# Kernel optimization log

Measured on AMD Instinct MI355X. Metric: run time of the kernel, lower is better.

The kernel has to match this reference:

```python
import jax, jax.numpy as jnp
import numpy as np

H = 4096          # hidden_size
I = 11008         # intermediate_size
G = 128           # AWQ group_size
# AWQ interleaved nibble order within each packed int32
_ORDER = jnp.array([0, 4, 1, 5, 2, 6, 3, 7], dtype=jnp.int32) * 4


def _mk_lin(key, K, N):
    k1, k2, k3 = jax.random.split(key, 3)
    qw = jax.random.randint(k1, (K, N // 8), 0, 100, dtype=jnp.int32)
    qz = jax.random.randint(k2, (K // G, N // 8), 0, 100, dtype=jnp.int32)
    sc = jax.random.normal(k3, (K // G, N), dtype=jnp.float32) * 0.02
    return qw, qz, sc


def setup_inputs() -> dict:
    key = jax.random.key(0)
    ks = jax.random.split(key, 7)
    x = jax.random.normal(ks[0], (8, 16, H), dtype=jnp.float32)
    ln1_w = jnp.ones((H,), dtype=jnp.float32)
    ln2_w = jnp.ones((H,), dtype=jnp.float32)
    qkv_qw, qkv_qz, qkv_sc = _mk_lin(ks[1], H, 3 * H)
    o_qw, o_qz, o_sc = _mk_lin(ks[2], H, H)
    gu_qw, gu_qz, gu_sc = _mk_lin(ks[3], H, 2 * I)
    dn_qw, dn_qz, dn_sc = _mk_lin(ks[4], I, H)
    return dict(x=x, ln1_w=ln1_w, ln2_w=ln2_w,
                qkv_qw=qkv_qw, qkv_qz=qkv_qz, qkv_sc=qkv_sc,
                o_qw=o_qw, o_qz=o_qz, o_sc=o_sc,
                gu_qw=gu_qw, gu_qz=gu_qz, gu_sc=gu_sc,
                dn_qw=dn_qw, dn_qz=dn_qz, dn_sc=dn_sc)


def rmsnorm(x, w, eps=1e-6):
    return x * jax.lax.rsqrt(jnp.mean(x * x, axis=-1, keepdims=True) + eps) * w


def dequant(qw, qz, sc):
    # qw: [K, N//8] int32 -> [K, N]; qz: [K//G, N//8] -> [K//G, N]
    K = qw.shape[0]
    N = sc.shape[1]
    w = ((qw[:, :, None] >> _ORDER) & 0xF).reshape(K, N).astype(sc.dtype)
    z = ((qz[:, :, None] >> _ORDER) & 0xF).reshape(K // G, N).astype(sc.dtype)
    return (w - jnp.repeat(z, G, axis=0)) * jnp.repeat(sc, G, axis=0)


def lite_linear(x, qw, qz, sc):
    return x @ dequant(qw, qz, sc)


def reference(x, ln1_w, ln2_w,
              qkv_qw, qkv_qz, qkv_sc,
              o_qw, o_qz, o_sc,
              gu_qw, gu_qz, gu_sc,
              dn_qw, dn_qz, dn_sc):
    residual = x
    h = rmsnorm(x, ln1_w)
    h = lite_linear(h, qkv_qw, qkv_qz, qkv_sc)[..., :H]  # mock attn: take q slice
    h = lite_linear(h, o_qw, o_qz, o_sc)
    h = residual + h
    residual = h
    h = rmsnorm(h, ln2_w)
    gate_up = lite_linear(h, gu_qw, gu_qz, gu_sc)
    gate, up = gate_up[..., :I], gate_up[..., I:]
    h = lite_linear(jax.nn.silu(gate) * up, dn_qw, dn_qz, dn_sc)
    return residual + h
```

## Files before the change

kernel.cpp:

```cpp
#include <hip/hip_runtime.h>

typedef unsigned int   u32;
typedef unsigned short u16;

typedef _Float16 h2  __attribute__((ext_vector_type(2)));
typedef _Float16 h8  __attribute__((ext_vector_type(8)));
typedef float    f32x4 __attribute__((ext_vector_type(4)));

#define M_TOK 128

__device__ __forceinline__ u16 f2h_(float f) {
    _Float16 h = (_Float16)f; return __builtin_bit_cast(u16, h);
}
__device__ __forceinline__ float h2f_(u16 b) {
    _Float16 h = __builtin_bit_cast(_Float16, b); return (float)h;
}
__device__ __forceinline__ void acc8(uint4 v, float* s) {
#pragma unroll
    for (int i = 0; i < 4; ++i) {
        u32 w = ((const u32*)&v)[i];
        s[2 * i]     += h2f_((u16)(w & 0xFFFF));
        s[2 * i + 1] += h2f_((u16)(w >> 16));
    }
}


__launch_bounds__(256)
__global__ void rmsnorm_k(const float* __restrict__ in, const float* __restrict__ w,
                          u16* __restrict__ out) {
    const int row = blockIdx.x;
    const float* x = in + (size_t)row * 4096;
    float ss = 0.f;
#pragma unroll
    for (int j = 0; j < 16; ++j) {
        float v = x[threadIdx.x + 256 * j];
        ss += v * v;
    }
#pragma unroll
    for (int off = 32; off > 0; off >>= 1) ss += __shfl_down(ss, off, 64);
    __shared__ float ws4[4];
    if ((threadIdx.x & 63) == 0) ws4[threadIdx.x >> 6] = ss;
    __syncthreads();
    float total = ws4[0] + ws4[1] + ws4[2] + ws4[3];
    float r = rsqrtf(total * (1.f / 4096.f) + 1e-6f);
    const int mt = row >> 4, l16 = row & 15;
#pragma unroll
    for (int c2 = 0; c2 < 2; ++c2) {
        int c = threadIdx.x * 2 + c2;
        int kb = c >> 2, qq = c & 3;
        u16 o8[8];
#pragma unroll
        for (int j = 0; j < 8; ++j) {
            int i = c * 8 + j;
            o8[j] = f2h_(x[i] * r * w[i]);
        }
        *(uint4*)(out + ((size_t)(kb * 8 + mt) * 64 + qq * 16 + l16) * 8) = *(const uint4*)o8;
    }
}

__launch_bounds__(256, 2)
__global__ void gemm_awq(const u16* __restrict__ A, const int* __restrict__ qw,
                         const int* __restrict__ qz, const float* __restrict__ sc,
                         u16* __restrict__ part,
                         int qws, int scs, int N, int K, int kchunk) {
    __shared__ __align__(16) char ldsB[4 * 4608];

    const int tid = threadIdx.x, w = tid >> 6, lane = tid & 63;
    const int q = lane >> 4, l16 = lane & 15;
    const int n0w = blockIdx.x * 128 + w * 32;
    const int pc0 = n0w >> 3;
    const int kp = lane & 31, h = lane >> 5;
    const int sk = blockIdx.y, kc0 = sk * kchunk, kend = min(kc0 + kchunk, K);

    char* myB   = ldsB + w * 4608;
    char* wbase = myB + kp * 4;
    const u16* Ala = A + lane * 8;
    const int* qws_base = qw + pc0;

    f32x4 acc[8][2] = {};
    h2 mzv[8], s2v[8];
    const int SH[8] = {0, 16, 4, 20, 8, 24, 12, 28};

    auto ldraw = [&](int k0) -> uint4 {
        return *(const uint4*)(qws_base + (size_t)(k0 + lane) * qws);
    };
    auto route = [&](uint4 rv, u32* d) {
        const int i0 = kp * 8, i1 = i0 + 4;
        int b00 = __builtin_amdgcn_ds_bpermute(i0, (int)rv.x);
        int b10 = __builtin_amdgcn_ds_bpermute(i0, (int)rv.y);
        int b20 = __builtin_amdgcn_ds_bpermute(i0, (int)rv.z);
        int b30 = __builtin_amdgcn_ds_bpermute(i0, (int)rv.w);
        int b01 = __builtin_amdgcn_ds_bpermute(i1, (int)rv.x);
        int b11 = __builtin_amdgcn_ds_bpermute(i1, (int)rv.y);
        int b21 = __builtin_amdgcn_ds_bpermute(i1, (int)rv.z);
        int b31 = __builtin_amdgcn_ds_bpermute(i1, (int)rv.w);
        d[0] = (u32)(h ? b10 : b00);
        d[1] = (u32)(h ? b11 : b01);
        d[2] = (u32)(h ? b30 : b20);
        d[3] = (u32)(h ? b31 : b21);
    };
    auto conv = [&](u32 z, const float* s8) {
#pragma unroll
        for (int j = 0; j < 8; ++j) {
            u32 zj = (z >> SH[j]) & 15u;
            mzv[j] = __builtin_bit_cast(h2, 0xE400E400u | zj | (zj << 16));
            _Float16 hs = (_Float16)s8[j];
            s2v[j] = (h2){hs, hs};
        }
    };
    auto emit8 = [&](u32 w0, u32 w1, int nb) {
        char* bb = wbase + nb * 144;
        u32 w0s = w0 >> 4, w1s = w1 >> 4;
        auto em = [&](int j, u32 a0, u32 a1, int b) {
            u32 t = __builtin_amdgcn_perm(a1, a0, (u32)(b | ((b + 4) << 16)));
            u32 u = (t & 0x000F000Fu) | 0x64006400u;
            h2 v = (__builtin_bit_cast(h2, u) + mzv[j]) * s2v[j];
            *(u32*)(bb + j * 144) = __builtin_bit_cast(u32, v);
        };
        em(0, w0, w1, 0);  em(4, w0, w1, 1);  em(1, w0, w1, 2);  em(5, w0, w1, 3);
        em(2, w0s, w1s, 0); em(6, w0s, w1s, 1); em(3, w0s, w1s, 2); em(7, w0s, w1s, 3);
    };

    const int pA = pc0 + h, pB = pc0 + h + 2;

    uint4 rv_c = ldraw(kc0);
    uint4 rv_n = {0, 0, 0, 0};
    if (kc0 + 64 < kend) rv_n = ldraw(kc0 + 64);
    {
        int g = kc0 >> 7;
        u32 z0 = (u32)qz[(size_t)g * qws + pA], z1 = (u32)qz[(size_t)g * qws + pB];
        const float* sb = sc + (size_t)g * scs + n0w + h * 8;
        float s8a[8], s8b[8];
        *(float4*)&s8a[0] = *(const float4*)sb;        *(float4*)&s8a[4] = *(const float4*)(sb + 4);
        *(float4*)&s8b[0] = *(const float4*)(sb + 16); *(float4*)&s8b[4] = *(const float4*)(sb + 20);
        u32 qc[4];
        route(rv_c, qc);
        conv(z0, s8a); emit8(qc[0], qc[1], h * 8);
        conv(z1, s8b); emit8(qc[2], qc[3], 16 + h * 8);
    }

    for (int k0 = kc0; k0 < kend; k0 += 64) {
        const bool kn1 = (k0 + 64) < kend, kn2 = (k0 + 128) < kend;
        u32 z0 = 0, z1 = 0; float s8a[8], s8b[8];
        if (kn1) {
            int g = (k0 + 64) >> 7;
            z0 = (u32)qz[(size_t)g * qws + pA]; z1 = (u32)qz[(size_t)g * qws + pB];
            const float* sb = sc + (size_t)g * scs + n0w + h * 8;
            *(float4*)&s8a[0] = *(const float4*)sb;        *(float4*)&s8a[4] = *(const float4*)(sb + 4);
            *(float4*)&s8b[0] = *(const float4*)(sb + 16); *(float4*)&s8b[4] = *(const float4*)(sb + 20);
        }
        uint4 af[2][8];
        const int kb0 = k0 >> 5;
#pragma unroll
        for (int c = 0; c < 2; ++c)
#pragma unroll
            for (int mt = 0; mt < 8; ++mt)
                af[c][mt] = *(const uint4*)(Ala + (size_t)((kb0 + c) * 8 + mt) * 512);
        uint4 bv[2][2];
#pragma unroll
        for (int c = 0; c < 2; ++c)
#pragma unroll
            for (int nt = 0; nt < 2; ++nt)
                bv[c][nt] = *(const uint4*)(myB + (nt * 16 + l16) * 144 + c * 64 + q * 16);
        uint4 rv_f = {0, 0, 0, 0};
        if (kn2) rv_f = ldraw(k0 + 128);
        if (kn1) {
            u32 qn[4];
            route(rv_n, qn);
            conv(z0, s8a); emit8(qn[0], qn[1], h * 8);
            conv(z1, s8b); emit8(qn[2], qn[3], 16 + h * 8);
        }
#pragma unroll
        for (int c = 0; c < 2; ++c)
#pragma unroll
            for (int mt = 0; mt < 8; ++mt)
#pragma unroll
                for (int nt = 0; nt < 2; ++nt)
                    acc[mt][nt] = __builtin_amdgcn_mfma_f32_16x16x32_f16(
                        __builtin_bit_cast(h8, af[c][mt]),
                        __builtin_bit_cast(h8, bv[c][nt]),
                        acc[mt][nt], 0, 0, 0);
        rv_n = rv_f;
    }

    u16* pp = part + (size_t)sk * M_TOK * N;
#pragma unroll
    for (int mt = 0; mt < 8; ++mt)
#pragma unroll
        for (int nt = 0; nt < 2; ++nt) {
            const int n = n0w + nt * 16 + l16;
#pragma unroll
            for (int r = 0; r < 4; ++r) {
                const int m = mt * 16 + q * 4 + r;
                pp[(size_t)m * N + n] = f2h_(acc[mt][nt][r]);
            }
        }
}

__launch_bounds__(256)
__global__ void reduce_to_afrag(const u16* __restrict__ part, u16* __restrict__ out,
                                int SK) {
    const int idx = blockIdx.x * 256 + threadIdx.x;
    const int m = idx >> 9, c = idx & 511;
    float s[8] = {};
    for (int k = 0; k < SK; ++k)
        acc8(*(const uint4*)(part + (size_t)k * 524288 + (size_t)m * 4096 + c * 8), s);
    const int kb = c >> 2, qq = c & 3, mt = m >> 4, l16 = m & 15;
    u16 o8[8];
#pragma unroll
    for (int j = 0; j < 8; ++j) o8[j] = f2h_(s[j]);
    *(uint4*)(out + ((size_t)(kb * 8 + mt) * 64 + qq * 16 + l16) * 8) = *(const uint4*)o8;
}

__launch_bounds__(256)
__global__ void reduce_add_f32(const u16* __restrict__ part, const float* __restrict__ resin,
                               float* __restrict__ out, int SK) {
    const int idx = blockIdx.x * 256 + threadIdx.x;
    const size_t base = (size_t)idx * 8;
    float s[8];
    *(float4*)&s[0] = *(const float4*)(resin + base);
    *(float4*)&s[4] = *(const float4*)(resin + base + 4);
    for (int k = 0; k < SK; ++k)
        acc8(*(const uint4*)(part + (size_t)k * 524288 + base), s);
    *(float4*)(out + base)     = *(const float4*)&s[0];
    *(float4*)(out + base + 4) = *(const float4*)&s[4];
}

__launch_bounds__(256)
__global__ void silu_mul(const u16* __restrict__ part, u16* __restrict__ act) {
    const int idx = blockIdx.x * 256 + threadIdx.x;
    const int m = idx / 1376, c = idx - m * 1376;
    const int nb = c * 8;
    float g[8] = {}, u[8] = {};
    for (int k = 0; k < 3; ++k) {
        const size_t base = (size_t)k * 2818048 + (size_t)m * 22016 + nb;
        acc8(*(const uint4*)(part + base), g);
        acc8(*(const uint4*)(part + base + 11008), u);
    }
    const int kb = nb >> 5, qq = (nb >> 3) & 3, mt = m >> 4, l16 = m & 15;
    u16 o8[8];
#pragma unroll
    for (int j = 0; j < 8; ++j) {
        float a = g[j] / (1.f + __expf(-g[j])) * u[j];
        o8[j] = f2h_(a);
    }
    *(uint4*)(act + ((size_t)(kb * 8 + mt) * 64 + qq * 16 + l16) * 8) = *(const uint4*)o8;
}

extern "C" void kernel_launch(void* const* d_in, const int* in_sizes, int n_in,
                              void* d_out, int out_size, void* d_ws, size_t ws_size,
                              hipStream_t stream) {
    const float* x      = (const float*)d_in[0];
    const float* ln1_w  = (const float*)d_in[1];
    const float* ln2_w  = (const float*)d_in[2];
    const int*   qkv_qw = (const int*)d_in[3];
    const int*   qkv_qz = (const int*)d_in[4];
    const float* qkv_sc = (const float*)d_in[5];
    const int*   o_qw   = (const int*)d_in[6];
    const int*   o_qz   = (const int*)d_in[7];
    const float* o_sc   = (const float*)d_in[8];
    const int*   gu_qw  = (const int*)d_in[9];
    const int*   gu_qz  = (const int*)d_in[10];
    const float* gu_sc  = (const float*)d_in[11];
    const int*   dn_qw  = (const int*)d_in[12];
    const int*   dn_qz  = (const int*)d_in[13];
    const float* dn_sc  = (const float*)d_in[14];
    float* out = (float*)d_out;

    char* ws = (char*)d_ws;
    u16*   pbuf = (u16*)(ws);
    u16*   act  = (u16*)(ws + 16908288);
    float* res2 = (float*)(ws + 19726336);
    u16*   slot = (u16*)(ws + 21823488);

    rmsnorm_k<<<128, 256, 0, stream>>>(x, ln1_w, slot);

    gemm_awq<<<dim3(32, 16), 256, 0, stream>>>(slot, qkv_qw, qkv_qz, qkv_sc, pbuf,
                                               1536, 12288, 4096, 4096, 256);
    reduce_to_afrag<<<256, 256, 0, stream>>>(pbuf, slot, 16);

    gemm_awq<<<dim3(32, 16), 256, 0, stream>>>(slot, o_qw, o_qz, o_sc, pbuf,
                                               512, 4096, 4096, 4096, 256);
    reduce_add_f32<<<256, 256, 0, stream>>>(pbuf, x, res2, 16);

    rmsnorm_k<<<128, 256, 0, stream>>>(res2, ln2_w, slot);

    gemm_awq<<<dim3(172, 3), 256, 0, stream>>>(slot, gu_qw, gu_qz, gu_sc, pbuf,
                                               2752, 22016, 22016, 4096, 1408);
    silu_mul<<<688, 256, 0, stream>>>(pbuf, act);

    gemm_awq<<<dim3(32, 16), 256, 0, stream>>>(act, dn_qw, dn_qz, dn_sc, pbuf,
                                               512, 4096, 4096, 11008, 704);
    reduce_add_f32<<<256, 256, 0, stream>>>(pbuf, res2, out, 16);
}
```

Before: 317.9 us.

## Prepack zero/scale pairs per layer and double-buffer A fragment loads

Adds a pack_zs kernel before each GEMM that turns the AWQ zero nibbles and fp32 scales into one u32 per column, holding a (-1024-z) half and a half scale. The GEMM then loads these packed pairs with vector loads only at group boundaries and extracts them with byte permutes, replacing per-step scalar qz and float4 scale loads plus conversion. A-fragment loads are also double-buffered across k-steps, so the next tile's loads are issued before the current MFMAs. This costs four extra small launches, extra workspace traffic and higher register pressure from the two A fragment buffers.

Measured after the change: 304.0 us. 1.05x faster.

```diff
diff --git a/kernel.cpp b/kernel.cpp
--- a/kernel.cpp
+++ b/kernel.cpp
@@ -22,6 +22,21 @@
         s[2 * i]     += h2f_((u16)(w & 0xFFFF));
         s[2 * i + 1] += h2f_((u16)(w >> 16));
     }
+}
+
+__constant__ int SHC[8] = {0, 16, 4, 20, 8, 24, 12, 28};
+
+__launch_bounds__(256)
+__global__ void pack_zs(const int* __restrict__ qz, const float* __restrict__ sc,
+                        u32* __restrict__ zs, int qws, int scs, int Ncols, int total) {
+    const int idx = blockIdx.x * 256 + threadIdx.x;
+    if (idx >= total) return;
+    const int g = idx / Ncols, n = idx - g * Ncols;
+    const u32 d = (u32)qz[(size_t)g * qws + (n >> 3)];
+    const u32 zj = (d >> SHC[n & 7]) & 15u;
+    const u32 mz = 0xE400u | zj;
+    const u16 sh = f2h_(sc[(size_t)g * scs + n]);
+    zs[(size_t)g * Ncols + n] = mz | ((u32)sh << 16);
 }
 
 
@@ -59,10 +74,9 @@
 }
 
 __launch_bounds__(256, 2)
-__global__ void gemm_awq(const u16* __restrict__ A, const int* __restrict__ qw,
-                         const int* __restrict__ qz, const float* __restrict__ sc,
-                         u16* __restrict__ part,
-                         int qws, int scs, int N, int K, int kchunk) {
+__global__ void gemm_awq(const u16* __restrict__ A, const u32* __restrict__ zs,
+                         const int* __restrict__ qw, u16* __restrict__ part,
+                         int qws, int N, int K, int kchunk) {
     __shared__ __align__(16) char ldsB[4 * 4608];
 
     const int tid = threadIdx.x, w = tid >> 6, lane = tid & 63;
@@ -76,13 +90,20 @@
     char* wbase = myB + kp * 4;
     const u16* Ala = A + lane * 8;
     const int* qws_base = qw + pc0;
+    const u32* zsA = zs + n0w + h * 8;
+    const u32* zsB = zs + n0w + 16 + h * 8;
 
     f32x4 acc[8][2] = {};
-    h2 mzv[8], s2v[8];
-    const int SH[8] = {0, 16, 4, 20, 8, 24, 12, 28};
+    uint4 za0, za1, zb0, zb1;
 
     auto ldraw = [&](int k0) -> uint4 {
         return *(const uint4*)(qws_base + (size_t)(k0 + lane) * qws);
+    };
+    auto loadzs = [&](int g) {
+        za0 = *(const uint4*)(zsA + (size_t)g * N);
+        za1 = *(const uint4*)(zsA + (size_t)g * N + 4);
+        zb0 = *(const uint4*)(zsB + (size_t)g * N);
+        zb1 = *(const uint4*)(zsB + (size_t)g * N + 4);
     };
     auto route = [&](uint4 rv, u32* d) {
         const int i0 = kp * 8, i1 = i0 + 4;
@@ -99,77 +120,66 @@
         d[2] = (u32)(h ? b30 : b20);
         d[3] = (u32)(h ? b31 : b21);
     };
-    auto conv = [&](u32 z, const float* s8) {
-#pragma unroll
-        for (int j = 0; j < 8; ++j) {
-            u32 zj = (z >> SH[j]) & 15u;
-            mzv[j] = __builtin_bit_cast(h2, 0xE400E400u | zj | (zj << 16));
-            _Float16 hs = (_Float16)s8[j];
-            s2v[j] = (h2){hs, hs};
-        }
-    };
-    auto emit8 = [&](u32 w0, u32 w1, int nb) {
+    auto emit8 = [&](u32 w0, u32 w1, int nb, uint4 z0, uint4 z1) {
         char* bb = wbase + nb * 144;
         u32 w0s = w0 >> 4, w1s = w1 >> 4;
-        auto em = [&](int j, u32 a0, u32 a1, int b) {
+        auto em = [&](int j, u32 a0, u32 a1, int b, u32 zsj) {
+            h2 mz = __builtin_bit_cast(h2, __builtin_amdgcn_perm(zsj, zsj, 0x01000100u));
+            h2 s2 = __builtin_bit_cast(h2, __builtin_amdgcn_perm(zsj, zsj, 0x03020302u));
             u32 t = __builtin_amdgcn_perm(a1, a0, (u32)(b | ((b + 4) << 16)));
             u32 u = (t & 0x000F000Fu) | 0x64006400u;
-            h2 v = (__builtin_bit_cast(h2, u) + mzv[j]) * s2v[j];
+            h2 v = (__builtin_bit_cast(h2, u) + mz) * s2;
             *(u32*)(bb + j * 144) = __builtin_bit_cast(u32, v);
         };
-        em(0, w0, w1, 0);  em(4, w0, w1, 1);  em(1, w0, w1, 2);  em(5, w0, w1, 3);
-        em(2, w0s, w1s, 0); em(6, w0s, w1s, 1); em(3, w0s, w1s, 2); em(7, w0s, w1s, 3);
-    };
-
-    const int pA = pc0 + h, pB = pc0 + h + 2;
-
-    uint4 rv_c = ldraw(kc0);
-    uint4 rv_n = {0, 0, 0, 0};
+        em(0, w0, w1, 0, z0.x);  em(4, w0, w1, 1, z1.x);
+        em(1, w0, w1, 2, z0.y);  em(5, w0, w1, 3, z1.y);
+        em(2, w0s, w1s, 0, z0.z); em(6, w0s, w1s, 1, z1.z);
+        em(3, w0s, w1s, 2, z0.w); em(7, w0s, w1s, 3, z1.w);
+    };
+    auto lda = [&](int k, uint4(&dst)[2][8]) {
+        const int kb = k >> 5;
+#pragma unroll
+        for (int c = 0; c < 2; ++c)
+#pragma unroll
+            for (int mt = 0; mt < 8; ++mt)
+                dst[c][mt] = *(const uint4*)(Ala + (size_t)((kb + c) * 8 + mt) * 512);
+    };
+
+    uint4 afA[2][8], afB[2][8];
+    uint4 rv_n = {0,0,0,0};
+
+    loadzs(kc0 >> 7);
+    uint4 rv0 = ldraw(kc0);
     if (kc0 + 64 < kend) rv_n = ldraw(kc0 + 64);
+    lda(kc0, afA);
     {
-        int g = kc0 >> 7;
-        u32 z0 = (u32)qz[(size_t)g * qws + pA], z1 = (u32)qz[(size_t)g * qws + pB];
-        const float* sb = sc + (size_t)g * scs + n0w + h * 8;
-        float s8a[8], s8b[8];
-        *(float4*)&s8a[0] = *(const float4*)sb;        *(float4*)&s8a[4] = *(const float4*)(sb + 4);
-        *(float4*)&s8b[0] = *(const float4*)(sb + 16); *(float4*)&s8b[4] = *(const float4*)(sb + 20);
-        u32 qc[4];
-        route(rv_c, qc);
-        conv(z0, s8a); emit8(qc[0], qc[1], h * 8);
-        conv(z1, s8b); emit8(qc[2], qc[3], 16 + h * 8);
-    }
-
-    for (int k0 = kc0; k0 < kend; k0 += 64) {
+        u32 qd[4];
+        route(rv0, qd);
+        emit8(qd[0], qd[1], h * 8, za0, za1);
+        emit8(qd[2], qd[3], 16 + h * 8, zb0, zb1);
+    }
+    if (((kc0 + 64) & 127) == 0 && kc0 + 64 < kend)
+        loadzs((kc0 + 64) >> 7);
+
+    auto step = [&](int k0, uint4(&cur)[2][8], uint4(&nxt)[2][8]) {
         const bool kn1 = (k0 + 64) < kend, kn2 = (k0 + 128) < kend;
-        u32 z0 = 0, z1 = 0; float s8a[8], s8b[8];
-        if (kn1) {
-            int g = (k0 + 64) >> 7;
-            z0 = (u32)qz[(size_t)g * qws + pA]; z1 = (u32)qz[(size_t)g * qws + pB];
-            const float* sb = sc + (size_t)g * scs + n0w + h * 8;
-            *(float4*)&s8a[0] = *(const float4*)sb;        *(float4*)&s8a[4] = *(const float4*)(sb + 4);
-            *(float4*)&s8b[0] = *(const float4*)(sb + 16); *(float4*)&s8b[4] = *(const float4*)(sb + 20);
-        }
-        uint4 af[2][8];
-        const int kb0 = k0 >> 5;
-#pragma unroll
-        for (int c = 0; c < 2; ++c)
-#pragma unroll
-            for (int mt = 0; mt < 8; ++mt)
-                af[c][mt] = *(const uint4*)(Ala + (size_t)((kb0 + c) * 8 + mt) * 512);
+        if (kn1) lda(k0 + 64, nxt);
         uint4 bv[2][2];
 #pragma unroll
         for (int c = 0; c < 2; ++c)
 #pragma unroll
             for (int nt = 0; nt < 2; ++nt)
                 bv[c][nt] = *(const uint4*)(myB + (nt * 16 + l16) * 144 + c * 64 + q * 16);
-        uint4 rv_f = {0, 0, 0, 0};
+        uint4 rv_f = {0,0,0,0};
         if (kn2) rv_f = ldraw(k0 + 128);
         if (kn1) {
-            u32 qn[4];
-            route(rv_n, qn);
-            conv(z0, s8a); emit8(qn[0], qn[1], h * 8);
-            conv(z1, s8b); emit8(qn[2], qn[3], 16 + h * 8);
+            u32 qd[4];
+            route(rv_n, qd);
+            emit8(qd[0], qd[1], h * 8, za0, za1);
+            emit8(qd[2], qd[3], 16 + h * 8, zb0, zb1);
         }
+        if (kn2 && (((k0 + 128) & 127) == 0))
+            loadzs((k0 + 128) >> 7);
 #pragma unroll
         for (int c = 0; c < 2; ++c)
 #pragma unroll
@@ -177,10 +187,14 @@
 #pragma unroll
                 for (int nt = 0; nt < 2; ++nt)
                     acc[mt][nt] = __builtin_amdgcn_mfma_f32_16x16x32_f16(
-                        __builtin_bit_cast(h8, af[c][mt]),
+                        __builtin_bit_cast(h8, cur[c][mt]),
                         __builtin_bit_cast(h8, bv[c][nt]),
                         acc[mt][nt], 0, 0, 0);
         rv_n = rv_f;
+    };
+    for (int k0 = kc0; k0 < kend; k0 += 128) {
+        step(k0, afA, afB);
+        if (k0 + 64 < kend) step(k0 + 64, afB, afA);
     }
 
     u16* pp = part + (size_t)sk * M_TOK * N;
@@ -269,27 +283,32 @@
 
     char* ws = (char*)d_ws;
     u16*   pbuf = (u16*)(ws);
-    u16*   act  = (u16*)(ws + 16908288);
-    float* res2 = (float*)(ws + 19726336);
-    u16*   slot = (u16*)(ws + 21823488);
+    u32*   zsb  = (u32*)(ws + 16908288);
+    u16*   act  = (u16*)(ws + 19726336);
+    float* res2 = (float*)(ws + 22544384);
+    u16*   slot = (u16*)(ws + 24641536);
 
     rmsnorm_k<<<128, 256, 0, stream>>>(x, ln1_w, slot);
-
-    gemm_awq<<<dim3(32, 16), 256, 0, stream>>>(slot, qkv_qw, qkv_qz, qkv_sc, pbuf,
-                                               1536, 12288, 4096, 4096, 256);
+    pack_zs<<<512, 256, 0, stream>>>(qkv_qz, qkv_sc, zsb, 1536, 12288, 4096, 131072);
+
+    gemm_awq<<<dim3(32, 16), 256, 0, stream>>>(slot, zsb, qkv_qw, pbuf,
+                                               1536, 4096, 4096, 256);
     reduce_to_afrag<<<256, 256, 0, stream>>>(pbuf, slot, 16);
-
-    gemm_awq<<<dim3(32, 16), 256, 0, stream>>>(slot, o_qw, o_qz, o_sc, pbuf,
-                                               512, 4096, 4096, 4096, 256);
+    pack_zs<<<512, 256, 0, stream>>>(o_qz, o_sc, zsb, 512, 4096, 4096, 131072);
+
+    gemm_awq<<<dim3(32, 16), 256, 0, stream>>>(slot, zsb, o_qw, pbuf,
+                                               512, 4096, 4096, 256);
     reduce_add_f32<<<256, 256, 0, stream>>>(pbuf, x, res2, 16);
 
     rmsnorm_k<<<128, 256, 0, stream>>>(res2, ln2_w, slot);
-
-    gemm_awq<<<dim3(172, 3), 256, 0, stream>>>(slot, gu_qw, gu_qz, gu_sc, pbuf,
-                                               2752, 22016, 22016, 4096, 1408);
+    pack_zs<<<2752, 256, 0, stream>>>(gu_qz, gu_sc, zsb, 2752, 22016, 22016, 704512);
+
+    gemm_awq<<<dim3(172, 3), 256, 0, stream>>>(slot, zsb, gu_qw, pbuf,
+                                               2752, 22016, 4096, 1408);
     silu_mul<<<688, 256, 0, stream>>>(pbuf, act);
-
-    gemm_awq<<<dim3(32, 16), 256, 0, stream>>>(act, dn_qw, dn_qz, dn_sc, pbuf,
-                                               512, 4096, 4096, 11008, 704);
+    pack_zs<<<1376, 256, 0, stream>>>(dn_qz, dn_sc, zsb, 512, 4096, 4096, 352256);
+
+    gemm_awq<<<dim3(32, 16), 256, 0, stream>>>(act, zsb, dn_qw, pbuf,
+                                               512, 4096, 11008, 704);
     reduce_add_f32<<<256, 256, 0, stream>>>(pbuf, res2, out, 16);
 }
```
